# Kernel optimization log

Measured on AMD Instinct MI355X. Metric: run time of the kernel, lower is better.

Reference implementation:

```python
import jax, jax.numpy as jnp
import numpy as np

S, B, C = 7, 2, 20
LAMBDA_COORD = 5.0
LAMBDA_NOOBJ = 0.5
WH_EPS = 1e-6
IOU_EPS = 1e-6
BATCH = 16384


def _iou_yolo(a, b):
    # a, b: [..., 4] in (cx, cy, w, h) 'yolo' center format
    ax1, ay1 = a[..., 0] - a[..., 2] / 2, a[..., 1] - a[..., 3] / 2
    ax2, ay2 = a[..., 0] + a[..., 2] / 2, a[..., 1] + a[..., 3] / 2
    bx1, by1 = b[..., 0] - b[..., 2] / 2, b[..., 1] - b[..., 3] / 2
    bx2, by2 = b[..., 0] + b[..., 2] / 2, b[..., 1] + b[..., 3] / 2
    iw = jnp.clip(jnp.minimum(ax2, bx2) - jnp.maximum(ax1, bx1), 0.0)
    ih = jnp.clip(jnp.minimum(ay2, by2) - jnp.maximum(ay1, by1), 0.0)
    inter = iw * ih
    area_a = jnp.abs((ax2 - ax1) * (ay2 - ay1))
    area_b = jnp.abs((bx2 - bx1) * (by2 - by1))
    return inter / (area_a + area_b - inter + IOU_EPS)


def setup_inputs() -> dict:
    key = jax.random.key(0)
    k1, k2, k3 = jax.random.split(key, 3)
    D = C + 5 * B  # 30
    y_trues = jax.random.uniform(k1, (BATCH, S, S, D), dtype=jnp.float32)
    # conf channel must be exactly 0.0 or 1.0 (loss branches on == 1)
    conf = (jax.random.uniform(k2, (BATCH, S, S)) < 0.3).astype(jnp.float32)
    y_trues = y_trues.at[..., 4].set(conf)
    y_preds = jax.random.normal(k3, (BATCH, S, S, D), dtype=jnp.float32)
    return {"y_trues": y_trues, "y_preds": y_preds}


def reference(y_trues, y_preds):
    D = C + 5 * B
    t = y_trues.reshape(-1, S * S, D)   # [N, 49, 30]
    p = y_preds.reshape(-1, S * S, D)
    batch_size = p.shape[0]

    b = t[..., 0:4]
    bhat1 = p[..., 0:4]
    bhat2 = p[..., 5:9]

    iou1 = _iou_yolo(b, bhat1)          # [N, 49]
    iou2 = _iou_yolo(b, bhat2)
    use1 = iou1 > iou2

    bhat = jnp.where(use1[..., None], bhat1, bhat2)            # responsible box
    confhat_chosen = jnp.where(use1, p[..., 4], p[..., 9])
    confhat_other = jnp.where(use1, p[..., 9], p[..., 4])

    # coord losses (object cells)
    xy = LAMBDA_COORD * ((b[..., 0] - bhat[..., 0]) ** 2 + (b[..., 1] - bhat[..., 1]) ** 2)
    wh = LAMBDA_COORD * (
        (jnp.sqrt(b[..., 2]) - jnp.sqrt(jnp.abs(bhat[..., 2] + WH_EPS))) ** 2
        + (jnp.sqrt(b[..., 3]) - jnp.sqrt(jnp.abs(bhat[..., 3] + WH_EPS))) ** 2
    )
    obj_conf = (t[..., 4] - confhat_chosen) ** 2
    noobj_in_obj = LAMBDA_NOOBJ * (0.0 - confhat_other) ** 2
    cls = jnp.sum((t[..., 10:] - p[..., 10:]) ** 2, axis=-1)

    obj_terms = xy + wh + obj_conf + noobj_in_obj + cls

    # no-object cells: penalize both predicted confs toward y_true conf (== target conf channel)
    noobj_terms = LAMBDA_NOOBJ * (
        (t[..., 4] - p[..., 4]) ** 2 + (t[..., 4] - p[..., 9]) ** 2
    )

    obj_mask = t[..., 4] == 1.0
    total = jnp.sum(jnp.where(obj_mask, obj_terms, noobj_terms))
    return total / batch_size
```

## Files before the change

kernel.cpp:

```cpp
#include <hip/hip_runtime.h>

#define LAMBDA_COORD 5.0f
#define LAMBDA_NOOBJ 0.5f
#define WH_EPS 1e-6f
#define IOU_EPS 1e-6f

constexpr int CHUNK_CELLS = 128;
constexpr int CHUNK_VEC4  = 960;
constexpr int NLOADS      = 15;
constexpr int GRID        = 1280;

__device__ __forceinline__ float iou_yolo(float a0, float a1, float a2, float a3,
                                          float b0, float b1, float b2, float b3) {
    float ax1 = a0 - a2 * 0.5f, ay1 = a1 - a3 * 0.5f;
    float ax2 = a0 + a2 * 0.5f, ay2 = a1 + a3 * 0.5f;
    float bx1 = b0 - b2 * 0.5f, by1 = b1 - b3 * 0.5f;
    float bx2 = b0 + b2 * 0.5f, by2 = b1 + b3 * 0.5f;
    float iw = fmaxf(fminf(ax2, bx2) - fmaxf(ax1, bx1), 0.0f);
    float ih = fmaxf(fminf(ay2, by2) - fmaxf(ay1, by1), 0.0f);
    float inter = iw * ih;
    float area_a = fabsf((ax2 - ax1) * (ay2 - ay1));
    float area_b = fabsf((bx2 - bx1) * (by2 - by1));
    return inter / (area_a + area_b - inter + IOU_EPS);
}

__device__ __forceinline__ float cell_loss(const float* t, const float* p) {
    const float b0 = t[0], b1 = t[1], b2 = t[2], b3 = t[3], t4 = t[4];

    float iou1 = iou_yolo(b0, b1, b2, b3, p[0], p[1], p[2], p[3]);
    float iou2 = iou_yolo(b0, b1, b2, b3, p[5], p[6], p[7], p[8]);
    bool use1 = iou1 > iou2;

    float bh0 = use1 ? p[0] : p[5];
    float bh1 = use1 ? p[1] : p[6];
    float bh2 = use1 ? p[2] : p[7];
    float bh3 = use1 ? p[3] : p[8];
    float conf_c = use1 ? p[4] : p[9];
    float conf_o = use1 ? p[9] : p[4];

    float dx = b0 - bh0, dy = b1 - bh1;
    float xy = LAMBDA_COORD * (dx * dx + dy * dy);

    float sw = sqrtf(b2) - sqrtf(fabsf(bh2 + WH_EPS));
    float sh = sqrtf(b3) - sqrtf(fabsf(bh3 + WH_EPS));
    float wh = LAMBDA_COORD * (sw * sw + sh * sh);

    float dc = t4 - conf_c;
    float obj_conf = dc * dc;
    float noobj_in_obj = LAMBDA_NOOBJ * conf_o * conf_o;

    float cls = 0.0f;
#pragma unroll
    for (int k = 10; k < 30; ++k) {
        float d = t[k] - p[k];
        cls += d * d;
    }

    float obj_terms = xy + wh + obj_conf + noobj_in_obj + cls;

    float d4 = t4 - p[4], d9 = t4 - p[9];
    float noobj_terms = LAMBDA_NOOBJ * (d4 * d4 + d9 * d9);

    return (t4 == 1.0f) ? obj_terms : noobj_terms;
}

__device__ __forceinline__ void stage16(const float4* g_wave, float4* l_wave, int lane) {
    __builtin_amdgcn_global_load_lds(
        (const __attribute__((address_space(1))) void*)(g_wave + lane),
        (__attribute__((address_space(3))) void*)l_wave,
        16, 0, 0);
}

__global__ __launch_bounds__(64) void yolo_loss_kernel(
    const float4* __restrict__ tv, const float4* __restrict__ pv,
    float* __restrict__ out, int nchunks, float inv_batch) {
    __shared__ float4 st4[CHUNK_VEC4];
    __shared__ float4 sp4[CHUNK_VEC4];
    const float* st = (const float*)st4;
    const float* sp = (const float*)sp4;

    const int lane = threadIdx.x;

    float v = 0.0f;

    for (int chunk = blockIdx.x; chunk < nchunks; chunk += GRID) {
        const float4* tg = tv + (size_t)chunk * CHUNK_VEC4;
        const float4* pg = pv + (size_t)chunk * CHUNK_VEC4;

#pragma unroll
        for (int j = 0; j < NLOADS; ++j)
            stage16(tg + j * 64, st4 + j * 64, lane);
#pragma unroll
        for (int j = 0; j < NLOADS; ++j)
            stage16(pg + j * 64, sp4 + j * 64, lane);

        __builtin_amdgcn_s_waitcnt(0x0F70);

        v += cell_loss(st + lane * 30, sp + lane * 30);
        v += cell_loss(st + (lane + 64) * 30, sp + (lane + 64) * 30);

        __builtin_amdgcn_s_waitcnt(0xC07F);
    }

#pragma unroll
    for (int off = 32; off > 0; off >>= 1)
        v += __shfl_down(v, off, 64);

    if (lane == 0) atomicAdd(out, v * inv_batch);
}

extern "C" void kernel_launch(void* const* d_in, const int* in_sizes, int n_in,
                              void* d_out, int out_size, void* d_ws, size_t ws_size,
                              hipStream_t stream) {
    const float* t = (const float*)d_in[0];
    const float* p = (const float*)d_in[1];
    float* out = (float*)d_out;

    const int total = in_sizes[0];
    const int cells = total / 30;
    const int nchunks = cells / CHUNK_CELLS;
    const int batch = cells / 49;
    const float inv_batch = 1.0f / (float)batch;

    hipMemsetAsync(out, 0, sizeof(float), stream);

    yolo_loss_kernel<<<GRID, 64, 0, stream>>>(
        (const float4*)t, (const float4*)p, out, nchunks, inv_batch);
}
```

Measured before the change: 207.6 us.

## Double-buffer LDS staging to prefetch the next chunk during compute

Halves the chunk size to 64 cells, one per lane, and adds a two-slot LDS buffer. While the current chunk is being computed, the asynchronous global-to-LDS loads for the next chunk are already in flight. A partial vmcnt wait then blocks only until the current chunk's loads have landed. The aim is to hide global memory latency behind the per-cell loss math. The cost is twice as many loop iterations and a lane-divergent tail load per array.

```diff
diff --git a/kernel.cpp b/kernel.cpp
--- a/kernel.cpp
+++ b/kernel.cpp
@@ -5,9 +5,8 @@
 #define WH_EPS 1e-6f
 #define IOU_EPS 1e-6f
 
-constexpr int CHUNK_CELLS = 128;
-constexpr int CHUNK_VEC4  = 960;
-constexpr int NLOADS      = 15;
+constexpr int CHUNK_CELLS = 64;
+constexpr int CHUNK_VEC4  = CHUNK_CELLS * 30/4;
 constexpr int GRID        = 1280;
 
 __device__ __forceinline__ float iou_yolo(float a0, float a1, float a2, float a3,
@@ -71,35 +70,49 @@
         16, 0, 0);
 }
 
+__device__ __forceinline__ void issue_array(const float4* g, float4* l, int lane) {
+#pragma unroll
+    for (int j = 0; j < 7; ++j)
+        stage16(g + j * 64, l + j * 64, lane);
+    if (lane < 32)
+        stage16(g + 7 * 64, l + 7 * 64, lane);
+}
+
 __global__ __launch_bounds__(64) void yolo_loss_kernel(
     const float4* __restrict__ tv, const float4* __restrict__ pv,
     float* __restrict__ out, int nchunks, float inv_batch) {
-    __shared__ float4 st4[CHUNK_VEC4];
-    __shared__ float4 sp4[CHUNK_VEC4];
-    const float* st = (const float*)st4;
-    const float* sp = (const float*)sp4;
+    __shared__ float4 sbuf[2][2][CHUNK_VEC4];
 
     const int lane = threadIdx.x;
 
     float v = 0.0f;
+    int g = blockIdx.x;
+    int parity = 0;
 
-    for (int chunk = blockIdx.x; chunk < nchunks; chunk += GRID) {
-        const float4* tg = tv + (size_t)chunk * CHUNK_VEC4;
-        const float4* pg = pv + (size_t)chunk * CHUNK_VEC4;
+    if (g < nchunks) {
+        issue_array(tv + (size_t)g * CHUNK_VEC4, sbuf[0][0], lane);
+        issue_array(pv + (size_t)g * CHUNK_VEC4, sbuf[0][1], lane);
+    }
 
-#pragma unroll
-        for (int j = 0; j < NLOADS; ++j)
-            stage16(tg + j * 64, st4 + j * 64, lane);
-#pragma unroll
-        for (int j = 0; j < NLOADS; ++j)
-            stage16(pg + j * 64, sp4 + j * 64, lane);
+    while (g < nchunks) {
+        const int gn = g + GRID;
+        const bool have_next = gn < nchunks;
+        if (have_next) {
+            issue_array(tv + (size_t)gn * CHUNK_VEC4, sbuf[1 - parity][0], lane);
+            issue_array(pv + (size_t)gn * CHUNK_VEC4, sbuf[1 - parity][1], lane);
+            __builtin_amdgcn_s_waitcnt(0x4F70);
+        } else {
+            __builtin_amdgcn_s_waitcnt(0x0F70);
+        }
 
-        __builtin_amdgcn_s_waitcnt(0x0F70);
-
+        const float* st = (const float*)sbuf[parity][0];
+        const float* sp = (const float*)sbuf[parity][1];
         v += cell_loss(st + lane * 30, sp + lane * 30);
-        v += cell_loss(st + (lane + 64) * 30, sp + (lane + 64) * 30);
 
         __builtin_amdgcn_s_waitcnt(0xC07F);
+
+        parity = 1 - parity;
+        g = gn;
     }
 
 #pragma unroll
```

Result: no change. 206.6 us (-0.5%).
